# Kernel optimization log

Measured on AMD Instinct MI355X. Metric: run time of the kernel, lower is better.

The kernel has to match this reference:

```python
import jax, jax.numpy as jnp
import numpy as np

EMBED_DIM = 1024
NUM_HEADS = 16
HEAD_DIM = EMBED_DIM // NUM_HEADS


def setup_inputs() -> dict:
    key = jax.random.key(0)
    ks = jax.random.split(key, 9)
    B, S, D = 2, 2048, EMBED_DIM
    s = 1.0 / np.sqrt(D)
    x = jax.random.normal(ks[0], (B, S, D), dtype=jnp.float32)
    Wq = jax.random.uniform(ks[1], (D, D), jnp.float32, -s, s)
    bq = jax.random.uniform(ks[2], (D,), jnp.float32, -s, s)
    Wk = jax.random.uniform(ks[3], (D, D), jnp.float32, -s, s)
    bk = jax.random.uniform(ks[4], (D,), jnp.float32, -s, s)
    Wv = jax.random.uniform(ks[5], (D, D), jnp.float32, -s, s)
    bv = jax.random.uniform(ks[6], (D,), jnp.float32, -s, s)
    Wo = jax.random.uniform(ks[7], (D, D), jnp.float32, -s, s)
    bo = jax.random.uniform(ks[8], (D,), jnp.float32, -s, s)
    return {"x": x, "Wq": Wq, "bq": bq, "Wk": Wk, "bk": bk,
            "Wv": Wv, "bv": bv, "Wo": Wo, "bo": bo}


def reference(x, Wq, bq, Wk, bk, Wv, bv, Wo, bo):
    B, S, D = x.shape
    H, Hd = NUM_HEADS, HEAD_DIM
    # projections (torch Linear: y = x W^T + b); split heads -> [B, H, S, Hd]
    def split(t):
        return t.reshape(B, S, H, Hd).transpose(0, 2, 1, 3)
    Q = split(x @ Wq.T + bq)
    K = split(x @ Wk.T + bk)
    V = split(x @ Wv.T + bv)
    scores = jnp.einsum('bhqd,bhkd->bhqk', Q, K) / jnp.sqrt(jnp.float32(Hd))
    weights = jax.nn.softmax(scores, axis=-1)
    out = jnp.einsum('bhqk,bhkd->bhqd', weights, V)
    out = out.transpose(0, 2, 1, 3).reshape(B, S, D)
    return out @ Wo.T + bo
```

## Files before the change

kernel.cpp:

```cpp
#include <hip/hip_runtime.h>

typedef float f32x4  __attribute__((ext_vector_type(4)));
typedef float f32x16 __attribute__((ext_vector_type(16)));
typedef short bh8    __attribute__((ext_vector_type(8)));
typedef unsigned int u32;

#define MFMA16(a, b, c) __builtin_amdgcn_mfma_f32_16x16x32_bf16(a, b, c, 0, 0, 0)
#define MFMA32(a, b, c) __builtin_amdgcn_mfma_f32_32x32x16_bf16(a, b, c, 0, 0, 0)

#define BB 2
#define SS 2048
#define DD 1024
#define HH 16
#define HDIM 64
#define TT (BB * SS)

#define QSCALE 0.18033688011f

__device__ __forceinline__ unsigned short f2bf(float f) {
  unsigned u = __float_as_uint(f);
  u += 0x7fffu + ((u >> 16) & 1u);
  return (unsigned short)(u >> 16);
}
__device__ __forceinline__ float bf2f(short h) {
  return __uint_as_float(((u32)(unsigned short)h) << 16);
}
__device__ __forceinline__ u32 cvtpk(float lo, float hi) {
  u32 r;
  asm("v_cvt_pk_bf16_f32 %0, %1, %2" : "=v"(r) : "v"(lo), "v"(hi));
  return r;
}
#define PLSWAP(a, b) \
  asm("v_permlane32_swap_b32 %0, %1" : "+v"(a), "+v"(b))

__device__ __forceinline__ void gload_lds16(const void* gsrc, const void* ldst) {
  __builtin_amdgcn_global_load_lds(
      (const __attribute__((address_space(1))) unsigned int*)(unsigned long long)gsrc,
      (__attribute__((address_space(3))) unsigned int*)(unsigned int)(unsigned long long)ldst,
      16, 0, 0);
}

__global__ void cvt_f32_bf16(const float* __restrict__ src,
                             unsigned short* __restrict__ dst, int n8) {
  int i = blockIdx.x * blockDim.x + threadIdx.x;
  if (i >= n8) return;
  const float4* s = (const float4*)src;
  float4 a = s[i * 2 + 0];
  float4 b = s[i * 2 + 1];
  bh8 v;
  v[0] = (short)f2bf(a.x); v[1] = (short)f2bf(a.y);
  v[2] = (short)f2bf(a.z); v[3] = (short)f2bf(a.w);
  v[4] = (short)f2bf(b.x); v[5] = (short)f2bf(b.y);
  v[6] = (short)f2bf(b.z); v[7] = (short)f2bf(b.w);
  *(bh8*)(dst + (size_t)i * 8) = v;
}

__global__ void cvt_w4(const float* __restrict__ w0, const float* __restrict__ w1,
                       const float* __restrict__ w2, const float* __restrict__ w3,
                       unsigned short* __restrict__ dst) {
  const int z = blockIdx.y;
  const float* src = (z == 0) ? w0 : (z == 1) ? w1 : (z == 2) ? w2 : w3;
  int i = blockIdx.x * blockDim.x + threadIdx.x;
  const float4* s = (const float4*)src;
  float4 a = s[i * 2 + 0];
  float4 b = s[i * 2 + 1];
  bh8 v;
  v[0] = (short)f2bf(a.x); v[1] = (short)f2bf(a.y);
  v[2] = (short)f2bf(a.z); v[3] = (short)f2bf(a.w);
  v[4] = (short)f2bf(b.x); v[5] = (short)f2bf(b.y);
  v[6] = (short)f2bf(b.z); v[7] = (short)f2bf(b.w);
  *(bh8*)(dst + (size_t)z * 1048576 + (size_t)i * 8) = v;
}

template <int EPI>
__global__ __launch_bounds__(256) void gemm128(
    const unsigned short* __restrict__ A,
    const unsigned short* __restrict__ Bw,
    const float* __restrict__ b0, const float* __restrict__ b1,
    const float* __restrict__ b2,
    unsigned short* __restrict__ Qw, unsigned short* __restrict__ Kw,
    unsigned short* __restrict__ Vtw, float* __restrict__ outf) {
  __shared__ __attribute__((aligned(16))) unsigned short As[128 * 32];
  __shared__ __attribute__((aligned(16))) unsigned short Bs[128 * 32];

  const int tid = threadIdx.x, lane = tid & 63, wid = tid >> 6;
  const int c = lane & 15, g = lane >> 4;
  const int wr = wid >> 1, wc = wid & 1;
  const int m0 = blockIdx.x * 128, n0 = blockIdx.y * 128;

  const unsigned short* Ab = A + (size_t)(m0 + (lane >> 2)) * DD + (lane & 3) * 8;
  const unsigned short* Bb = Bw + (size_t)(n0 + (lane >> 2)) * DD + (lane & 3) * 8;

  f32x4 acc[4][4];
#pragma unroll
  for (int mi = 0; mi < 4; ++mi)
#pragma unroll
    for (int ni = 0; ni < 4; ++ni) acc[mi][ni] = (f32x4){0.f, 0.f, 0.f, 0.f};

  for (int k0 = 0; k0 < DD; k0 += 32) {
    __syncthreads();
#pragma unroll
    for (int r = 0; r < 2; ++r) {
      const int rowb = wid * 32 + r * 16;
      gload_lds16(Ab + (size_t)rowb * DD + k0, &As[rowb * 32]);
      gload_lds16(Bb + (size_t)rowb * DD + k0, &Bs[rowb * 32]);
    }
    __syncthreads();

    bh8 a[4], b[4];
#pragma unroll
    for (int mi = 0; mi < 4; ++mi)
      a[mi] = *(const bh8*)&As[(wr * 64 + mi * 16 + c) * 32 + g * 8];
#pragma unroll
    for (int ni = 0; ni < 4; ++ni)
      b[ni] = *(const bh8*)&Bs[(wc * 64 + ni * 16 + c) * 32 + g * 8];
#pragma unroll
    for (int mi = 0; mi < 4; ++mi)
#pragma unroll
      for (int ni = 0; ni < 4; ++ni)
        acc[mi][ni] = MFMA16(a[mi], b[ni], acc[mi][ni]);
  }

  if (EPI == 0) {
#pragma unroll
    for (int ni = 0; ni < 4; ++ni) {
      const int n = n0 + wc * 64 + ni * 16 + c;
      const int z = n >> 10, oo = n & 1023;
      const float bias = (z == 0 ? b0 : (z == 1 ? b1 : b2))[oo];
      const int h = oo >> 6, hd = oo & 63;
#pragma unroll
      for (int mi = 0; mi < 4; ++mi)
#pragma unroll
        for (int j = 0; j < 4; ++j) {
          const int m = m0 + wr * 64 + mi * 16 + g * 4 + j;
          const int bb = m >> 11, s = m & (SS - 1);
          float vv = acc[mi][ni][j] + bias;
          if (z == 0) vv *= QSCALE;
          const unsigned short v = f2bf(vv);
          if (z == 2)
            Vtw[(((size_t)(bb * HH + h) * HDIM + hd) << 11) + s] = v;
          else {
            unsigned short* O = (z == 0) ? Qw : Kw;
            O[(((size_t)(bb * HH + h) * SS + s) << 6) + hd] = v;
          }
        }
    }
  } else {
#pragma unroll
    for (int ni = 0; ni < 4; ++ni) {
      const int n = n0 + wc * 64 + ni * 16 + c;
      const float bias = b0[n];
#pragma unroll
      for (int mi = 0; mi < 4; ++mi)
#pragma unroll
        for (int j = 0; j < 4; ++j) {
          const int m = m0 + wr * 64 + mi * 16 + g * 4 + j;
          outf[(size_t)m * DD + n] = acc[mi][ni][j] + bias;
        }
    }
  }
}

__global__ __launch_bounds__(256, 3) void attn7(
    const unsigned short* __restrict__ Qw, const unsigned short* __restrict__ Kw,
    const unsigned short* __restrict__ Vtw,
    unsigned short* __restrict__ o0, unsigned short* __restrict__ o1,
    float* __restrict__ lbuf) {
  __shared__ __attribute__((aligned(16))) unsigned short KT[2][4096];
  __shared__ __attribute__((aligned(16))) unsigned short VT[2][4096];

  const int f = blockIdx.x;
  const int work = (f & 7) * 128 + (f >> 3);
  const int bx = work & 15;
  const int kvh = (work >> 4) & 1;
  const int bhh = work >> 5;
  const int by = bhh & 15, bz = bhh >> 4;

  const int tid = threadIdx.x;
  const int lane = tid & 63, wid = tid >> 6;
  const int q = lane & 31, hi = lane >> 5;
  const int x7 = lane & 7;
  const int bh = bz * HH + by;
  const unsigned short* Qb = Qw + (size_t)bh * SS * HDIM;
  const unsigned short* Kb = Kw + (size_t)bh * SS * HDIM + (size_t)kvh * 1024 * HDIM;
  const unsigned short* Vb = Vtw + (size_t)bh * HDIM * SS + (size_t)kvh * 1024;
  const int q0 = bx * 128 + wid * 32;

  bh8 qf[4];
#pragma unroll
  for (int ks = 0; ks < 4; ++ks)
    qf[ks] = *(const bh8*)(Qb + (size_t)(q0 + q) * HDIM + ks * 16 + hi * 8);

  f32x16 O0, O1;
#pragma unroll
  for (int r = 0; r < 16; ++r) { O0[r] = 0.f; O1[r] = 0.f; }
  float la[4] = {0.f, 0.f, 0.f, 0.f};

  const int srow = tid >> 2;
  const int c0 = (tid & 3) * 2;
  const int sr7 = srow & 7;
  const int wk0 = srow * 64 + ((c0) ^ sr7) * 8;
  const int wk1 = srow * 64 + ((c0 + 1) ^ sr7) * 8;
  const unsigned short* Ksrc = Kb + (size_t)srow * HDIM + c0 * 8;
  const unsigned short* Vsrc = Vb + (size_t)srow * SS + c0 * 8;

  bh8 kr0 = *(const bh8*)(Ksrc + 0), kr1 = *(const bh8*)(Ksrc + 8);
  bh8 vr0 = *(const bh8*)(Vsrc + 0), vr1 = *(const bh8*)(Vsrc + 8);
  *(bh8*)&KT[0][wk0] = kr0; *(bh8*)&KT[0][wk1] = kr1;
  *(bh8*)&VT[0][wk0] = vr0; *(bh8*)&VT[0][wk1] = vr1;
  kr0 = *(const bh8*)(Ksrc + 64 * HDIM); kr1 = *(const bh8*)(Ksrc + 64 * HDIM + 8);
  vr0 = *(const bh8*)(Vsrc + 64);        vr1 = *(const bh8*)(Vsrc + 64 + 8);

  const int NT = 1024 / 64;
  for (int kt = 0; kt < NT; ++kt) {
    const int cur = kt & 1;
    __syncthreads();
    if (kt + 1 < NT) {
      *(bh8*)&KT[cur ^ 1][wk0] = kr0;
      *(bh8*)&KT[cur ^ 1][wk1] = kr1;
      *(bh8*)&VT[cur ^ 1][wk0] = vr0;
      *(bh8*)&VT[cur ^ 1][wk1] = vr1;
      if (kt + 2 < NT) {
        const size_t ko = (size_t)(kt + 2) * 64 * HDIM, vo = (size_t)(kt + 2) * 64;
        kr0 = *(const bh8*)(Ksrc + ko); kr1 = *(const bh8*)(Ksrc + ko + 8);
        vr0 = *(const bh8*)(Vsrc + vo); vr1 = *(const bh8*)(Vsrc + vo + 8);
      }
    }

#pragma unroll
    for (int kvt = 0; kvt < 2; ++kvt) {
      bh8 kf[4];
#pragma unroll
      for (int ks = 0; ks < 4; ++ks)
        kf[ks] = *(const bh8*)&KT[cur][(kvt * 32 + q) * 64 +
                                       (((ks * 2 + hi) ^ x7) * 8)];
      f32x16 a;
#pragma unroll
      for (int r = 0; r < 16; ++r) a[r] = 0.f;
      __builtin_amdgcn_s_setprio(1);
#pragma unroll
      for (int ks = 0; ks < 4; ++ks) a = MFMA32(kf[ks], qf[ks], a);
      __builtin_amdgcn_s_setprio(0);

      bh8 vf00 = *(const bh8*)&VT[cur][q * 64 + (((kvt * 4 + hi) ^ x7) * 8)];
      bh8 vf01 = *(const bh8*)&VT[cur][(32 + q) * 64 + (((kvt * 4 + hi) ^ x7) * 8)];
      bh8 vf10 = *(const bh8*)&VT[cur][q * 64 + (((kvt * 4 + 2 + hi) ^ x7) * 8)];
      bh8 vf11 = *(const bh8*)&VT[cur][(32 + q) * 64 + (((kvt * 4 + 2 + hi) ^ x7) * 8)];

      u32 w[8];
#pragma unroll
      for (int i = 0; i < 8; ++i) {
        float p0 = __builtin_amdgcn_exp2f(a[2 * i]);
        float p1 = __builtin_amdgcn_exp2f(a[2 * i + 1]);
        la[i & 3] += p0 + p1;
        w[i] = cvtpk(p0, p1);
      }
      PLSWAP(w[0], w[2]); PLSWAP(w[1], w[3]);
      PLSWAP(w[4], w[6]); PLSWAP(w[5], w[7]);

      union { u32 uw[4]; bh8 h; } pa0, pa1;
#pragma unroll
      for (int j = 0; j < 4; ++j) { pa0.uw[j] = w[j]; pa1.uw[j] = w[4 + j]; }
      __builtin_amdgcn_s_setprio(1);
      O0 = MFMA32(vf00, pa0.h, O0);
      O1 = MFMA32(vf01, pa0.h, O1);
      O0 = MFMA32(vf10, pa1.h, O0);
      O1 = MFMA32(vf11, pa1.h, O1);
      __builtin_amdgcn_s_setprio(0);
    }
  }

  float l = (la[0] + la[1]) + (la[2] + la[3]);
  {
    float xa = l, xb = l;
    asm("" : "+v"(xb));
    PLSWAP(xa, xb);
    l = xa + xb;
  }
  if (hi == 0) lbuf[kvh * (BB * HH * SS) + bh * SS + q0 + q] = l;

  unsigned short* orow =
      (kvh ? o1 : o0) + (size_t)(bz * SS + q0 + q) * DD + by * HDIM;
#pragma unroll
  for (int rq = 0; rq < 4; ++rq) {
    const int db0 = 8 * rq + 4 * hi;
    uint2 v0, v1;
    v0.x = cvtpk(O0[4 * rq + 0], O0[4 * rq + 1]);
    v0.y = cvtpk(O0[4 * rq + 2], O0[4 * rq + 3]);
    v1.x = cvtpk(O1[4 * rq + 0], O1[4 * rq + 1]);
    v1.y = cvtpk(O1[4 * rq + 2], O1[4 * rq + 3]);
    *(uint2*)(orow + db0) = v0;
    *(uint2*)(orow + 32 + db0) = v1;
  }
}

__global__ __launch_bounds__(256) void attn_merge(
    const unsigned short* __restrict__ p0, const unsigned short* __restrict__ p1,
    const float* __restrict__ lbuf, unsigned short* outw) {
  const int i = blockIdx.x * blockDim.x + threadIdx.x;
  const int base = i * 8;
  const int row = base >> 10, col = base & 1023;
  const int li = (((row >> 11) << 4) + (col >> 6)) * SS + (row & (SS - 1));
  const float inv = 1.0f / (lbuf[li] + lbuf[BB * HH * SS + li]);
  bh8 a = *(const bh8*)(p0 + base);
  bh8 b = *(const bh8*)(p1 + base);
  bh8 o;
#pragma unroll
  for (int j = 0; j < 8; ++j)
    o[j] = (short)f2bf((bf2f(a[j]) + bf2f(b[j])) * inv);
  *(bh8*)(outw + base) = o;
}

extern "C" void kernel_launch(void* const* d_in, const int* in_sizes, int n_in,
                              void* d_out, int out_size, void* d_ws,
                              size_t ws_size, hipStream_t stream) {
  const float* x  = (const float*)d_in[0];
  const float* Wq = (const float*)d_in[1];
  const float* bq = (const float*)d_in[2];
  const float* Wk = (const float*)d_in[3];
  const float* bk = (const float*)d_in[4];
  const float* Wv = (const float*)d_in[5];
  const float* bv = (const float*)d_in[6];
  const float* Wo = (const float*)d_in[7];
  const float* bo = (const float*)d_in[8];
  float* out = (float*)d_out;

  unsigned short* ws = (unsigned short*)d_ws;
  unsigned short* xb    = ws;
  unsigned short* Wqb   = ws + 4194304;
  unsigned short* Qw    = ws + 8388608;
  unsigned short* Kw    = ws + 12582912;
  unsigned short* Vtw   = ws + 16777216;
  unsigned short* attnw = ws + 20971520;
  float* lbuf = (float*)(ws + 4194304);

  cvt_f32_bf16<<<(TT * DD / 8 + 255) / 256, 256, 0, stream>>>(x, xb, TT * DD / 8);
  cvt_w4<<<dim3(DD * DD / 8 / 256, 4), 256, 0, stream>>>(Wq, Wk, Wv, Wo, Wqb);

  gemm128<0><<<dim3(TT / 128, 3072 / 128), 256, 0, stream>>>(
      xb, Wqb, bq, bk, bv, Qw, Kw, Vtw, nullptr);

  attn7<<<dim3(1024), 256, 0, stream>>>(Qw, Kw, Vtw, attnw, xb, lbuf);
  attn_merge<<<dim3(TT * DD / 8 / 256), 256, 0, stream>>>(attnw, xb, lbuf, attnw);

  gemm128<1><<<dim3(TT / 128, DD / 128), 256, 0, stream>>>(
      attnw, Wqb + 3 * 1048576, bo, nullptr, nullptr, nullptr, nullptr, nullptr, out);
}
```

Baseline: 120.5 us.

## Use single-wave attention blocks reading K/V directly from global, merge conversion kernels

The attention kernel now runs one 64-lane wave per block and loads K and V fragments straight from global memory (relying on cache) instead of staging them through double-buffered shared memory with barriers. The grid grows to 4096 blocks to keep the same amount of work. This removes LDS traffic and __syncthreads but gives up K/V reuse across the four waves of a block, which raises L2 and global load pressure. Separately, the x and weight fp32-to-bf16 conversion kernels are merged into one launch to save launch overhead.

New measurement: 196.1 us. 1.63x slower.

```diff
diff --git a/kernel.cpp b/kernel.cpp
--- a/kernel.cpp
+++ b/kernel.cpp
@@ -40,36 +40,33 @@
       16, 0, 0);
 }
 
-__global__ void cvt_f32_bf16(const float* __restrict__ src,
-                             unsigned short* __restrict__ dst, int n8) {
-  int i = blockIdx.x * blockDim.x + threadIdx.x;
-  if (i >= n8) return;
+__global__ void cvt_all(const float* __restrict__ x,
+                        const float* __restrict__ w0, const float* __restrict__ w1,
+                        const float* __restrict__ w2, const float* __restrict__ w3,
+                        unsigned short* __restrict__ xb,
+                        unsigned short* __restrict__ wb) {
+  const int b = blockIdx.x;
+  const float* src;
+  unsigned short* dst;
+  int i;
+  if (b < 2048) {
+    src = x; dst = xb;
+    i = b * 256 + threadIdx.x;
+  } else {
+    const int z = (b - 2048) >> 9;
+    src = (z == 0) ? w0 : (z == 1) ? w1 : (z == 2) ? w2 : w3;
+    dst = wb + (size_t)z * 1048576;
+    i = ((b - 2048) & 511) * 256 + threadIdx.x;
+  }
   const float4* s = (const float4*)src;
   float4 a = s[i * 2 + 0];
-  float4 b = s[i * 2 + 1];
+  float4 c = s[i * 2 + 1];
   bh8 v;
   v[0] = (short)f2bf(a.x); v[1] = (short)f2bf(a.y);
   v[2] = (short)f2bf(a.z); v[3] = (short)f2bf(a.w);
-  v[4] = (short)f2bf(b.x); v[5] = (short)f2bf(b.y);
-  v[6] = (short)f2bf(b.z); v[7] = (short)f2bf(b.w);
+  v[4] = (short)f2bf(c.x); v[5] = (short)f2bf(c.y);
+  v[6] = (short)f2bf(c.z); v[7] = (short)f2bf(c.w);
   *(bh8*)(dst + (size_t)i * 8) = v;
-}
-
-__global__ void cvt_w4(const float* __restrict__ w0, const float* __restrict__ w1,
-                       const float* __restrict__ w2, const float* __restrict__ w3,
-                       unsigned short* __restrict__ dst) {
-  const int z = blockIdx.y;
-  const float* src = (z == 0) ? w0 : (z == 1) ? w1 : (z == 2) ? w2 : w3;
-  int i = blockIdx.x * blockDim.x + threadIdx.x;
-  const float4* s = (const float4*)src;
-  float4 a = s[i * 2 + 0];
-  float4 b = s[i * 2 + 1];
-  bh8 v;
-  v[0] = (short)f2bf(a.x); v[1] = (short)f2bf(a.y);
-  v[2] = (short)f2bf(a.z); v[3] = (short)f2bf(a.w);
-  v[4] = (short)f2bf(b.x); v[5] = (short)f2bf(b.y);
-  v[6] = (short)f2bf(b.z); v[7] = (short)f2bf(b.w);
-  *(bh8*)(dst + (size_t)z * 1048576 + (size_t)i * 8) = v;
 }
 
 template <int EPI>
@@ -161,30 +158,25 @@
   }
 }
 
-__global__ __launch_bounds__(256, 3) void attn7(
+__global__ __launch_bounds__(64, 4) void attn8(
     const unsigned short* __restrict__ Qw, const unsigned short* __restrict__ Kw,
     const unsigned short* __restrict__ Vtw,
     unsigned short* __restrict__ o0, unsigned short* __restrict__ o1,
     float* __restrict__ lbuf) {
-  __shared__ __attribute__((aligned(16))) unsigned short KT[2][4096];
-  __shared__ __attribute__((aligned(16))) unsigned short VT[2][4096];
-
   const int f = blockIdx.x;
-  const int work = (f & 7) * 128 + (f >> 3);
-  const int bx = work & 15;
-  const int kvh = (work >> 4) & 1;
-  const int bhh = work >> 5;
+  const int work = (f & 7) * 512 + (f >> 3);
+  const int bx = work & 63;
+  const int kvh = (work >> 6) & 1;
+  const int bhh = work >> 7;
   const int by = bhh & 15, bz = bhh >> 4;
 
-  const int tid = threadIdx.x;
-  const int lane = tid & 63, wid = tid >> 6;
+  const int lane = threadIdx.x;
   const int q = lane & 31, hi = lane >> 5;
-  const int x7 = lane & 7;
   const int bh = bz * HH + by;
   const unsigned short* Qb = Qw + (size_t)bh * SS * HDIM;
   const unsigned short* Kb = Kw + (size_t)bh * SS * HDIM + (size_t)kvh * 1024 * HDIM;
   const unsigned short* Vb = Vtw + (size_t)bh * HDIM * SS + (size_t)kvh * 1024;
-  const int q0 = bx * 128 + wid * 32;
+  const int q0 = bx * 32;
 
   bh8 qf[4];
 #pragma unroll
@@ -196,78 +188,48 @@
   for (int r = 0; r < 16; ++r) { O0[r] = 0.f; O1[r] = 0.f; }
   float la[4] = {0.f, 0.f, 0.f, 0.f};
 
-  const int srow = tid >> 2;
-  const int c0 = (tid & 3) * 2;
-  const int sr7 = srow & 7;
-  const int wk0 = srow * 64 + ((c0) ^ sr7) * 8;
-  const int wk1 = srow * 64 + ((c0 + 1) ^ sr7) * 8;
-  const unsigned short* Ksrc = Kb + (size_t)srow * HDIM + c0 * 8;
-  const unsigned short* Vsrc = Vb + (size_t)srow * SS + c0 * 8;
-
-  bh8 kr0 = *(const bh8*)(Ksrc + 0), kr1 = *(const bh8*)(Ksrc + 8);
-  bh8 vr0 = *(const bh8*)(Vsrc + 0), vr1 = *(const bh8*)(Vsrc + 8);
-  *(bh8*)&KT[0][wk0] = kr0; *(bh8*)&KT[0][wk1] = kr1;
-  *(bh8*)&VT[0][wk0] = vr0; *(bh8*)&VT[0][wk1] = vr1;
-  kr0 = *(const bh8*)(Ksrc + 64 * HDIM); kr1 = *(const bh8*)(Ksrc + 64 * HDIM + 8);
-  vr0 = *(const bh8*)(Vsrc + 64);        vr1 = *(const bh8*)(Vsrc + 64 + 8);
-
-  const int NT = 1024 / 64;
-  for (int kt = 0; kt < NT; ++kt) {
-    const int cur = kt & 1;
-    __syncthreads();
-    if (kt + 1 < NT) {
-      *(bh8*)&KT[cur ^ 1][wk0] = kr0;
-      *(bh8*)&KT[cur ^ 1][wk1] = kr1;
-      *(bh8*)&VT[cur ^ 1][wk0] = vr0;
-      *(bh8*)&VT[cur ^ 1][wk1] = vr1;
-      if (kt + 2 < NT) {
-        const size_t ko = (size_t)(kt + 2) * 64 * HDIM, vo = (size_t)(kt + 2) * 64;
-        kr0 = *(const bh8*)(Ksrc + ko); kr1 = *(const bh8*)(Ksrc + ko + 8);
-        vr0 = *(const bh8*)(Vsrc + vo); vr1 = *(const bh8*)(Vsrc + vo + 8);
-      }
+  const unsigned short* krow = Kb + (size_t)q * HDIM + hi * 8;
+  const unsigned short* vrow0 = Vb + (size_t)q * SS + hi * 8;
+  const unsigned short* vrow1 = Vb + (size_t)(32 + q) * SS + hi * 8;
+
+  for (int kv0 = 0; kv0 < 1024; kv0 += 32) {
+    bh8 kf[4];
+#pragma unroll
+    for (int ks = 0; ks < 4; ++ks)
+      kf[ks] = *(const bh8*)(krow + (size_t)kv0 * HDIM + ks * 16);
+    f32x16 a;
+#pragma unroll
+    for (int r = 0; r < 16; ++r) a[r] = 0.f;
+    __builtin_amdgcn_s_setprio(1);
+#pragma unroll
+    for (int ks = 0; ks < 4; ++ks) a = MFMA32(kf[ks], qf[ks], a);
+    __builtin_amdgcn_s_setprio(0);
+
+    bh8 vf00 = *(const bh8*)(vrow0 + kv0);
+    bh8 vf01 = *(const bh8*)(vrow1 + kv0);
+    bh8 vf10 = *(const bh8*)(vrow0 + kv0 + 16);
+    bh8 vf11 = *(const bh8*)(vrow1 + kv0 + 16);
+
+    u32 w[8];
+#pragma unroll
+    for (int i = 0; i < 8; ++i) {
+      float p0 = __builtin_amdgcn_exp2f(a[2 * i]);
+      float p1 = __builtin_amdgcn_exp2f(a[2 * i + 1]);
+      la[i & 3] += p0 + p1;
+      w[i] = cvtpk(p0, p1);
     }
-
-#pragma unroll
-    for (int kvt = 0; kvt < 2; ++kvt) {
-      bh8 kf[4];
-#pragma unroll
-      for (int ks = 0; ks < 4; ++ks)
-        kf[ks] = *(const bh8*)&KT[cur][(kvt * 32 + q) * 64 +
-                                       (((ks * 2 + hi) ^ x7) * 8)];
-      f32x16 a;
-#pragma unroll
-      for (int r = 0; r < 16; ++r) a[r] = 0.f;
-      __builtin_amdgcn_s_setprio(1);
-#pragma unroll
-      for (int ks = 0; ks < 4; ++ks) a = MFMA32(kf[ks], qf[ks], a);
-      __builtin_amdgcn_s_setprio(0);
-
-      bh8 vf00 = *(const bh8*)&VT[cur][q * 64 + (((kvt * 4 + hi) ^ x7) * 8)];
-      bh8 vf01 = *(const bh8*)&VT[cur][(32 + q) * 64 + (((kvt * 4 + hi) ^ x7) * 8)];
-      bh8 vf10 = *(const bh8*)&VT[cur][q * 64 + (((kvt * 4 + 2 + hi) ^ x7) * 8)];
-      bh8 vf11 = *(const bh8*)&VT[cur][(32 + q) * 64 + (((kvt * 4 + 2 + hi) ^ x7) * 8)];
-
-      u32 w[8];
-#pragma unroll
-      for (int i = 0; i < 8; ++i) {
-        float p0 = __builtin_amdgcn_exp2f(a[2 * i]);
-        float p1 = __builtin_amdgcn_exp2f(a[2 * i + 1]);
-        la[i & 3] += p0 + p1;
-        w[i] = cvtpk(p0, p1);
-      }
-      PLSWAP(w[0], w[2]); PLSWAP(w[1], w[3]);
-      PLSWAP(w[4], w[6]); PLSWAP(w[5], w[7]);
-
-      union { u32 uw[4]; bh8 h; } pa0, pa1;
-#pragma unroll
-      for (int j = 0; j < 4; ++j) { pa0.uw[j] = w[j]; pa1.uw[j] = w[4 + j]; }
-      __builtin_amdgcn_s_setprio(1);
-      O0 = MFMA32(vf00, pa0.h, O0);
-      O1 = MFMA32(vf01, pa0.h, O1);
-      O0 = MFMA32(vf10, pa1.h, O0);
-      O1 = MFMA32(vf11, pa1.h, O1);
-      __builtin_amdgcn_s_setprio(0);
-    }
+    PLSWAP(w[0], w[2]); PLSWAP(w[1], w[3]);
+    PLSWAP(w[4], w[6]); PLSWAP(w[5], w[7]);
+
+    union { u32 uw[4]; bh8 h; } pa0, pa1;
+#pragma unroll
+    for (int j = 0; j < 4; ++j) { pa0.uw[j] = w[j]; pa1.uw[j] = w[4 + j]; }
+    __builtin_amdgcn_s_setprio(1);
+    O0 = MFMA32(vf00, pa0.h, O0);
+    O1 = MFMA32(vf01, pa0.h, O1);
+    O0 = MFMA32(vf10, pa1.h, O0);
+    O1 = MFMA32(vf11, pa1.h, O1);
+    __builtin_amdgcn_s_setprio(0);
   }
 
   float l = (la[0] + la[1]) + (la[2] + la[3]);
@@ -334,13 +296,12 @@
   unsigned short* attnw = ws + 20971520;
   float* lbuf = (float*)(ws + 4194304);
 
-  cvt_f32_bf16<<<(TT * DD / 8 + 255) / 256, 256, 0, stream>>>(x, xb, TT * DD / 8);
-  cvt_w4<<<dim3(DD * DD / 8 / 256, 4), 256, 0, stream>>>(Wq, Wk, Wv, Wo, Wqb);
+  cvt_all<<<dim3(4096), 256, 0, stream>>>(x, Wq, Wk, Wv, Wo, xb, Wqb);
 
   gemm128<0><<<dim3(TT / 128, 3072 / 128), 256, 0, stream>>>(
       xb, Wqb, bq, bk, bv, Qw, Kw, Vtw, nullptr);
 
-  attn7<<<dim3(1024), 256, 0, stream>>>(Qw, Kw, Vtw, attnw, xb, lbuf);
+  attn8<<<dim3(4096), 64, 0, stream>>>(Qw, Kw, Vtw, attnw, xb, lbuf);
   attn_merge<<<dim3(TT * DD / 8 / 256), 256, 0, stream>>>(attnw, xb, lbuf, attnw);
 
   gemm128<1><<<dim3(TT / 128, DD / 128), 256, 0, stream>>>(
```

## Double-buffer GEMM LDS tiles with prefetch and merge conversion kernels

Applied to the files above, without the earlier changes.

The 128x128 bf16 GEMM now uses two LDS buffers per operand. It issues the async global-to-LDS loads for the next K-slice before running the MFMAs on the current one, so each iteration needs one barrier instead of two. MFMA issue priority is raised around the inner product with s_setprio. The separate input and weight f32-to-bf16 conversion kernels are merged into a single launch to cut launch overhead. The cost is twice the LDS per block, which may lower occupancy, and correctness relies on the barrier waiting for the outstanding async LDS loads.

After: 117.8 us. 2.2% less time.

```diff
diff --git a/kernel.cpp b/kernel.cpp
--- a/kernel.cpp
+++ b/kernel.cpp
@@ -40,36 +40,33 @@
       16, 0, 0);
 }
 
-__global__ void cvt_f32_bf16(const float* __restrict__ src,
-                             unsigned short* __restrict__ dst, int n8) {
-  int i = blockIdx.x * blockDim.x + threadIdx.x;
-  if (i >= n8) return;
+__global__ void cvt_all(const float* __restrict__ x,
+                        const float* __restrict__ w0, const float* __restrict__ w1,
+                        const float* __restrict__ w2, const float* __restrict__ w3,
+                        unsigned short* __restrict__ xb,
+                        unsigned short* __restrict__ wb) {
+  const int b = blockIdx.x;
+  const float* src;
+  unsigned short* dst;
+  int i;
+  if (b < 2048) {
+    src = x; dst = xb;
+    i = b * 256 + threadIdx.x;
+  } else {
+    const int z = (b - 2048) >> 9;
+    src = (z == 0) ? w0 : (z == 1) ? w1 : (z == 2) ? w2 : w3;
+    dst = wb + (size_t)z * 1048576;
+    i = ((b - 2048) & 511) * 256 + threadIdx.x;
+  }
   const float4* s = (const float4*)src;
   float4 a = s[i * 2 + 0];
-  float4 b = s[i * 2 + 1];
+  float4 c = s[i * 2 + 1];
   bh8 v;
   v[0] = (short)f2bf(a.x); v[1] = (short)f2bf(a.y);
   v[2] = (short)f2bf(a.z); v[3] = (short)f2bf(a.w);
-  v[4] = (short)f2bf(b.x); v[5] = (short)f2bf(b.y);
-  v[6] = (short)f2bf(b.z); v[7] = (short)f2bf(b.w);
+  v[4] = (short)f2bf(c.x); v[5] = (short)f2bf(c.y);
+  v[6] = (short)f2bf(c.z); v[7] = (short)f2bf(c.w);
   *(bh8*)(dst + (size_t)i * 8) = v;
-}
-
-__global__ void cvt_w4(const float* __restrict__ w0, const float* __restrict__ w1,
-                       const float* __restrict__ w2, const float* __restrict__ w3,
-                       unsigned short* __restrict__ dst) {
-  const int z = blockIdx.y;
-  const float* src = (z == 0) ? w0 : (z == 1) ? w1 : (z == 2) ? w2 : w3;
-  int i = blockIdx.x * blockDim.x + threadIdx.x;
-  const float4* s = (const float4*)src;
-  float4 a = s[i * 2 + 0];
-  float4 b = s[i * 2 + 1];
-  bh8 v;
-  v[0] = (short)f2bf(a.x); v[1] = (short)f2bf(a.y);
-  v[2] = (short)f2bf(a.z); v[3] = (short)f2bf(a.w);
-  v[4] = (short)f2bf(b.x); v[5] = (short)f2bf(b.y);
-  v[6] = (short)f2bf(b.z); v[7] = (short)f2bf(b.w);
-  *(bh8*)(dst + (size_t)z * 1048576 + (size_t)i * 8) = v;
 }
 
 template <int EPI>
@@ -80,8 +77,8 @@
     const float* __restrict__ b2,
     unsigned short* __restrict__ Qw, unsigned short* __restrict__ Kw,
     unsigned short* __restrict__ Vtw, float* __restrict__ outf) {
-  __shared__ __attribute__((aligned(16))) unsigned short As[128 * 32];
-  __shared__ __attribute__((aligned(16))) unsigned short Bs[128 * 32];
+  __shared__ __attribute__((aligned(16))) unsigned short As[2][128 * 32];
+  __shared__ __attribute__((aligned(16))) unsigned short Bs[2][128 * 32];
 
   const int tid = threadIdx.x, lane = tid & 63, wid = tid >> 6;
   const int c = lane & 15, g = lane >> 4;
@@ -90,6 +87,7 @@
 
   const unsigned short* Ab = A + (size_t)(m0 + (lane >> 2)) * DD + (lane & 3) * 8;
   const unsigned short* Bb = Bw + (size_t)(n0 + (lane >> 2)) * DD + (lane & 3) * 8;
+  const int rowb0 = wid * 32, rowb1 = wid * 32 + 16;
 
   f32x4 acc[4][4];
 #pragma unroll
@@ -97,28 +95,39 @@
 #pragma unroll
     for (int ni = 0; ni < 4; ++ni) acc[mi][ni] = (f32x4){0.f, 0.f, 0.f, 0.f};
 
-  for (int k0 = 0; k0 < DD; k0 += 32) {
-    __syncthreads();
-#pragma unroll
-    for (int r = 0; r < 2; ++r) {
-      const int rowb = wid * 32 + r * 16;
-      gload_lds16(Ab + (size_t)rowb * DD + k0, &As[rowb * 32]);
-      gload_lds16(Bb + (size_t)rowb * DD + k0, &Bs[rowb * 32]);
-    }
-    __syncthreads();
+  gload_lds16(Ab + (size_t)rowb0 * DD, &As[0][rowb0 * 32]);
+  gload_lds16(Ab + (size_t)rowb1 * DD, &As[0][rowb1 * 32]);
+  gload_lds16(Bb + (size_t)rowb0 * DD, &Bs[0][rowb0 * 32]);
+  gload_lds16(Bb + (size_t)rowb1 * DD, &Bs[0][rowb1 * 32]);
+  __syncthreads();
+
+  const int NT = DD / 32;
+  for (int t = 0; t < NT; ++t) {
+    const int cur = t & 1;
+    if (t + 1 < NT) {
+      const int k1 = (t + 1) * 32;
+      gload_lds16(Ab + (size_t)rowb0 * DD + k1, &As[cur ^ 1][rowb0 * 32]);
+      gload_lds16(Ab + (size_t)rowb1 * DD + k1, &As[cur ^ 1][rowb1 * 32]);
+      gload_lds16(Bb + (size_t)rowb0 * DD + k1, &Bs[cur ^ 1][rowb0 * 32]);
+      gload_lds16(Bb + (size_t)rowb1 * DD + k1, &Bs[cur ^ 1][rowb1 * 32]);
+    }
 
     bh8 a[4], b[4];
 #pragma unroll
     for (int mi = 0; mi < 4; ++mi)
-      a[mi] = *(const bh8*)&As[(wr * 64 + mi * 16 + c) * 32 + g * 8];
+      a[mi] = *(const bh8*)&As[cur][(wr * 64 + mi * 16 + c) * 32 + g * 8];
 #pragma unroll
     for (int ni = 0; ni < 4; ++ni)
-      b[ni] = *(const bh8*)&Bs[(wc * 64 + ni * 16 + c) * 32 + g * 8];
+      b[ni] = *(const bh8*)&Bs[cur][(wc * 64 + ni * 16 + c) * 32 + g * 8];
+    __builtin_amdgcn_s_setprio(1);
 #pragma unroll
     for (int mi = 0; mi < 4; ++mi)
 #pragma unroll
       for (int ni = 0; ni < 4; ++ni)
         acc[mi][ni] = MFMA16(a[mi], b[ni], acc[mi][ni]);
+    __builtin_amdgcn_s_setprio(0);
+
+    __syncthreads();
   }
 
   if (EPI == 0) {
@@ -334,8 +343,7 @@
   unsigned short* attnw = ws + 20971520;
   float* lbuf = (float*)(ws + 4194304);
 
-  cvt_f32_bf16<<<(TT * DD / 8 + 255) / 256, 256, 0, stream>>>(x, xb, TT * DD / 8);
-  cvt_w4<<<dim3(DD * DD / 8 / 256, 4), 256, 0, stream>>>(Wq, Wk, Wv, Wo, Wqb);
+  cvt_all<<<dim3(4096), 256, 0, stream>>>(x, Wq, Wk, Wv, Wo, xb, Wqb);
 
   gemm128<0><<<dim3(TT / 128, 3072 / 128), 256, 0, stream>>>(
       xb, Wqb, bq, bk, bv, Qw, Kw, Vtw, nullptr);
```
